# Optimization experiments

Hardware: AMD Instinct MI355X
Metric: run time of the kernel (lower is better)

The kernel has to match this reference:

```python
import jax, jax.numpy as jnp
import numpy as np

N, E, D, ED, L = 40000, 640000, 128, 16, 3  # nodes, edges, emb_dim, edge_dim, num_layer
BN_EPS = 1e-5


def setup_inputs() -> dict:
    key = jax.random.key(0)
    ks = jax.random.split(key, 20)
    s = 0.05
    inp = {
        "x": jax.random.normal(ks[0], (N, D), jnp.float32),
        "edge_attr": jax.random.normal(ks[1], (E, ED), jnp.float32),
        # node encoder Linear(input_dim, emb_dim)
        "node_W": jax.random.normal(ks[2], (D, D), jnp.float32) * s,
        "node_b": jnp.zeros((D,), jnp.float32),
        # per-layer params (leading dim L)
        "edge_W": jax.random.normal(ks[3], (L, ED, D), jnp.float32) * s,
        "edge_b": jnp.zeros((L, D), jnp.float32),
        "attn_W": jax.random.normal(ks[4], (L, 2 * D, 1), jnp.float32) * s,
        "attn_b": jnp.zeros((L, 1), jnp.float32),
        "eps": jnp.zeros((L,), jnp.float32),
        "W1": jax.random.normal(ks[5], (L, D, 2 * D), jnp.float32) * s,
        "b1": jnp.zeros((L, 2 * D), jnp.float32),
        "bn1_g": jnp.ones((L, 2 * D), jnp.float32),
        "bn1_b": jnp.zeros((L, 2 * D), jnp.float32),
        "W2": jax.random.normal(ks[6], (L, 2 * D, D), jnp.float32) * s,
        "b2": jnp.zeros((L, D), jnp.float32),
        "bn_g": jnp.ones((L, D), jnp.float32),
        "bn_b": jnp.zeros((L, D), jnp.float32),
        "edge_index": jax.random.randint(ks[7], (2, E), 0, N, jnp.int32),
    }
    return inp


def _bn_eval(h, g, b):
    # BatchNorm1d in eval with running_mean=0, running_var=1
    return g * h * (1.0 / np.sqrt(1.0 + BN_EPS)) + b


def reference(x, edge_attr, node_W, node_b, edge_W, edge_b, attn_W, attn_b,
              eps, W1, b1, bn1_g, bn1_b, W2, b2, bn_g, bn_b, edge_index):
    src, dst = edge_index[0], edge_index[1]
    h = x @ node_W + node_b  # node_encoder, [N, D]
    for l in range(L):
        e = edge_attr @ edge_W[l] + edge_b[l]       # [E, D] edge embedding
        xj = h[src]                                  # [E, D] source gather
        xi = h[dst]                                  # [E, D] target gather
        a = jax.nn.sigmoid(jnp.concatenate([xi, xj], axis=-1) @ attn_W[l] + attn_b[l])  # [E,1]
        msg = jax.nn.relu(xj * a + e)                # fused per-edge message
        agg = jax.ops.segment_sum(msg, dst, num_segments=N)  # scatter-add aggregate
        z = (1.0 + eps[l]) * h + agg
        # GIN mlp: Linear -> BN(eval) -> ReLU -> Linear
        z = _bn_eval(z @ W1[l] + b1[l], bn1_g[l], bn1_b[l])
        z = jax.nn.relu(z)
        z = z @ W2[l] + b2[l]
        # outer BatchNorm(eval); dropout = identity in eval; JK='last', no residual
        z = _bn_eval(z, bn_g[l], bn_b[l])
        if l < L - 1:
            z = jax.nn.relu(z)
        h = z
    return h
```

## Files before the change

kernel.cpp:

```cpp
#include <hip/hip_runtime.h>
#include <math.h>

#define NN 40000
#define EE 640000
#define DD 128
#define EDD 16
#define LL 3
#define TEB 64

__device__ __constant__ float kBnInv = 0.9999950000374997f;

typedef __bf16 bf16x8 __attribute__((ext_vector_type(8)));
typedef float  f32x4  __attribute__((ext_vector_type(4)));
typedef float  f32x2  __attribute__((ext_vector_type(2)));

__device__ __forceinline__ unsigned pack_bf2(float a, float b) {
    unsigned ua = __float_as_uint(a), ub = __float_as_uint(b);
    ua = (ua + 0x7fffu + ((ua >> 16) & 1u)) >> 16;
    ub = (ub + 0x7fffu + ((ub >> 16) & 1u)) & 0xffff0000u;
    return ua | ub;
}
__device__ __forceinline__ unsigned short bf16r(float x) {
    unsigned u = __float_as_uint(x);
    u = (u + 0x7fffu + ((u >> 16) & 1u)) >> 16;
    return (unsigned short)u;
}

__global__ __launch_bounds__(256) void node_enc_kernel(
    const float* __restrict__ x, const float* __restrict__ W,
    const float* __restrict__ b,
    const float* __restrict__ aW, const float* __restrict__ eps_p,
    float* __restrict__ h, unsigned* __restrict__ hb,
    float* __restrict__ pi, float* __restrict__ pj, float* __restrict__ z)
{
    __shared__ float xs[32][DD];
    const int t = threadIdx.x;
    const long rowbase = (long)blockIdx.x * 32;

    const float4* x4 = (const float4*)(x + rowbase * DD);
    float4* xs4 = (float4*)&xs[0][0];
#pragma unroll
    for (int i = 0; i < 4; i++) xs4[t + i * 256] = x4[t + i * 256];
    __syncthreads();

    const int c  = (t & 31) * 4;
    const int r0 = (t >> 5) * 4;

    float acc[4][4] = {};
    for (int k4 = 0; k4 < DD; k4 += 4) {
        float4 xr[4];
#pragma unroll
        for (int i = 0; i < 4; i++) xr[i] = *(const float4*)&xs[r0 + i][k4];
#pragma unroll
        for (int kk = 0; kk < 4; kk++) {
            const float4 w = *(const float4*)(W + (k4 + kk) * DD + c);
#pragma unroll
            for (int i = 0; i < 4; i++) {
                const float xv = ((const float*)&xr[i])[kk];
                acc[i][0] = fmaf(xv, w.x, acc[i][0]);
                acc[i][1] = fmaf(xv, w.y, acc[i][1]);
                acc[i][2] = fmaf(xv, w.z, acc[i][2]);
                acc[i][3] = fmaf(xv, w.w, acc[i][3]);
            }
        }
    }
    const float4 bv  = *(const float4*)(b + c);
    const float4 awi = *(const float4*)(aW + c);
    const float4 awj = *(const float4*)(aW + DD + c);
    const float ep = 1.0f + eps_p[0];

    float pa[4], pb[4];
#pragma unroll
    for (int i = 0; i < 4; i++) {
        const long row = rowbase + r0 + i;
        float4 ov = { acc[i][0] + bv.x, acc[i][1] + bv.y,
                      acc[i][2] + bv.z, acc[i][3] + bv.w };
        *(float4*)(h + row * DD + c) = ov;
        uint2 pv = { pack_bf2(ov.x, ov.y), pack_bf2(ov.z, ov.w) };
        *(uint2*)(hb + row * 64 + (c >> 1)) = pv;
        float4 zv = { ep * ov.x, ep * ov.y, ep * ov.z, ep * ov.w };
        *(float4*)(z + row * DD + c) = zv;
        pa[i] = ov.x * awi.x + ov.y * awi.y + ov.z * awi.z + ov.w * awi.w;
        pb[i] = ov.x * awj.x + ov.y * awj.y + ov.z * awj.z + ov.w * awj.w;
    }
#pragma unroll
    for (int off = 1; off < 32; off <<= 1) {
#pragma unroll
        for (int i = 0; i < 4; i++) {
            pa[i] += __shfl_xor(pa[i], off, 64);
            pb[i] += __shfl_xor(pb[i], off, 64);
        }
    }
    if ((t & 31) == 0) {
#pragma unroll
        for (int i = 0; i < 4; i++) {
            pi[rowbase + r0 + i] = pa[i];
            pj[rowbase + r0 + i] = pb[i];
        }
    }
}

__global__ __launch_bounds__(256) void wcast_kernel(
    const float* __restrict__ W1, const float* __restrict__ W2,
    unsigned short* __restrict__ w1t, unsigned short* __restrict__ w2t)
{
    const int idx = blockIdx.x * 256 + threadIdx.x;
    const int l = idx >> 15, r = idx & 32767;
    {   const int n = r >> 7, k = r & 127;
        w1t[idx] = bf16r(W1[(l << 15) + (k << 8) + n]);
    }
    {   const int n = r >> 8, k = r & 255;
        w2t[idx] = bf16r(W2[(l << 15) + (k << 7) + n]);
    }
}

__global__ __launch_bounds__(256) void hist_kernel(
    const int* __restrict__ edge_index, int* __restrict__ counts)
{
    const int i = blockIdx.x * 256 + threadIdx.x;
    atomicAdd(&counts[edge_index[EE + i]], 1);
}

__global__ __launch_bounds__(256) void scan1_kernel(
    const int* __restrict__ counts, int* __restrict__ scanned,
    int* __restrict__ partials)
{
    __shared__ int sdata[256];
    const int t = threadIdx.x;
    const int base = blockIdx.x * 1024 + t * 4;
    int v[4]; int sum = 0;
#pragma unroll
    for (int i = 0; i < 4; i++) {
        const int idx = base + i;
        v[i] = (idx < NN) ? counts[idx] : 0;
        sum += v[i];
    }
    sdata[t] = sum;
    __syncthreads();
    for (int off = 1; off < 256; off <<= 1) {
        int x = (t >= off) ? sdata[t - off] : 0;
        __syncthreads();
        sdata[t] += x;
        __syncthreads();
    }
    int run = sdata[t] - sum;
#pragma unroll
    for (int i = 0; i < 4; i++) {
        const int idx = base + i;
        if (idx < NN) scanned[idx] = run;
        run += v[i];
    }
    if (t == 255) partials[blockIdx.x] = sdata[255];
}

__global__ void scan2_kernel(int* __restrict__ partials)
{
    if (threadIdx.x == 0) {
        int run = 0;
        for (int i = 0; i < 40; i++) { int v = partials[i]; partials[i] = run; run += v; }
    }
}

__global__ __launch_bounds__(256) void scan3_kernel(
    const int* __restrict__ scanned, const int* __restrict__ partials,
    int* __restrict__ offsets, int* __restrict__ cursor)
{
    const int idx = blockIdx.x * 256 + threadIdx.x;
    if (idx < NN) {
        const int off = scanned[idx] + partials[idx >> 10];
        offsets[idx] = off;
        cursor[idx]  = off;
    }
}

__global__ __launch_bounds__(256) void scatter_kernel(
    const int* __restrict__ edge_index, const float* __restrict__ edge_attr,
    int* __restrict__ cursor,
    int* __restrict__ srcs_p, int* __restrict__ dstd_p,
    unsigned* __restrict__ ea_b)
{
    const int i = blockIdx.x * 256 + threadIdx.x;
    const int src = edge_index[i];
    const int dst = edge_index[EE + i];
    const int pos = atomicAdd(&cursor[dst], 1);
    srcs_p[pos] = src << 6;
    dstd_p[pos] = dst << 7;

    const float4* sp = (const float4*)(edge_attr + (long)i * EDD);
    const float4 s0 = sp[0], s1 = sp[1], s2 = sp[2], s3 = sp[3];
    uint4 o0 = { pack_bf2(s0.x, s0.y), pack_bf2(s0.z, s0.w),
                 pack_bf2(s1.x, s1.y), pack_bf2(s1.z, s1.w) };
    uint4 o1 = { pack_bf2(s2.x, s2.y), pack_bf2(s2.z, s2.w),
                 pack_bf2(s3.x, s3.y), pack_bf2(s3.z, s3.w) };
    *(uint4*)(ea_b + (long)pos * 8)     = o0;
    *(uint4*)(ea_b + (long)pos * 8 + 4) = o1;
}

__global__ __launch_bounds__(256) void edge_msg_kernel(
    const unsigned* __restrict__ hb, const unsigned* __restrict__ ea_b,
    const float* __restrict__ pi, const float* __restrict__ pj,
    const int* __restrict__ srcs_p, const int* __restrict__ dstd_p,
    const float* __restrict__ ab_p,
    const float* __restrict__ eW, const float* __restrict__ eb,
    float* __restrict__ z)
{
    __shared__ unsigned sh_hb[TEB * 64];
    __shared__ float    sh_ea[TEB * EDD];
    __shared__ int      sh_src[TEB];
    __shared__ int      sh_dst[TEB];
    __shared__ float    sh_a[TEB];

    const int t = threadIdx.x;
    const long e0 = (long)blockIdx.x * TEB;

    if (t < TEB) {
        const int ss = srcs_p[e0 + t];
        const int dd = dstd_p[e0 + t];
        sh_src[t] = ss;
        sh_dst[t] = dd;
        const float s = pi[dd >> 7] + pj[ss >> 6] + ab_p[0];
        sh_a[t] = 1.0f / (1.0f + expf(-s));
    }
    __syncthreads();

    {
        const int chunk = t & 15;
        const int r0    = t >> 4;
#pragma unroll
        for (int i = 0; i < TEB / 16; i++) {
            const int row  = r0 + 16 * i;
            const int srow = sh_src[row];
            *(uint4*)&sh_hb[row * 64 + chunk * 4] =
                *(const uint4*)(hb + srow + chunk * 4);
        }
#pragma unroll
        for (int i = 0; i < 2; i++) {
            const int idx  = t * 2 + i;
            const int edge = idx >> 3, q = idx & 7;
            const unsigned u = ea_b[e0 * 8 + idx];
            float2 f = { __uint_as_float(u << 16),
                         __uint_as_float(u & 0xffff0000u) };
            *(float2*)&sh_ea[edge * EDD + q * 2] = f;
        }
    }
    __syncthreads();

    const int wid = t >> 6, lane = t & 63;
    const int c0 = lane * 2;
    const int base = wid * (TEB / 4);

    f32x2 ew[EDD];
#pragma unroll
    for (int q = 0; q < EDD; q++) {
        const float2 w2 = ((const float2*)(eW + q * DD))[lane];
        ew[q][0] = w2.x; ew[q][1] = w2.y;
    }
    const float2 ebf = ((const float2*)eb)[lane];
    const f32x2 ebv = { ebf.x, ebf.y };
    const f32x2 zero2 = { 0.0f, 0.0f };

    f32x2 acc = zero2;
    int cur = sh_dst[base];

#pragma unroll 4
    for (int j = 0; j < TEB / 4; j++) {
        const int   dd = sh_dst[base + j];
        const float a  = sh_a[base + j];
        const unsigned u = sh_hb[(base + j) * 64 + lane];

        const float4* eap = (const float4*)&sh_ea[(base + j) * EDD];
        const float4 t0 = eap[0], t1 = eap[1], t2 = eap[2], t3 = eap[3];
        const float ea[EDD] = { t0.x,t0.y,t0.z,t0.w, t1.x,t1.y,t1.z,t1.w,
                                t2.x,t2.y,t2.z,t2.w, t3.x,t3.y,t3.z,t3.w };
        f32x2 ev = ebv;
#pragma unroll
        for (int q = 0; q < EDD; q++) {
            const f32x2 eaq = { ea[q], ea[q] };
            ev = __builtin_elementwise_fma(eaq, ew[q], ev);
        }

        if (dd != cur) {
            atomicAdd(&z[cur + c0],     acc[0]);
            atomicAdd(&z[cur + c0 + 1], acc[1]);
            acc = zero2; cur = dd;
        }
        const f32x2 xj = { __uint_as_float(u << 16),
                           __uint_as_float(u & 0xffff0000u) };
        const f32x2 av = { a, a };
        f32x2 m = __builtin_elementwise_fma(xj, av, ev);
        m = __builtin_elementwise_max(m, zero2);
        acc += m;
    }
    atomicAdd(&z[cur + c0],     acc[0]);
    atomicAdd(&z[cur + c0 + 1], acc[1]);
}

__global__ __launch_bounds__(256) void mlp_mfma_kernel(
    const float* __restrict__ zin,
    const unsigned short* __restrict__ w1t, const unsigned short* __restrict__ w2t,
    const float* __restrict__ b1, const float* __restrict__ g1, const float* __restrict__ bb1,
    const float* __restrict__ b2, const float* __restrict__ g2, const float* __restrict__ bb2,
    const float* __restrict__ aWn, const float* __restrict__ epsn_p,
    float* __restrict__ out, unsigned* __restrict__ hb,
    float* __restrict__ pi, float* __restrict__ pj, float* __restrict__ z,
    const int do_relu)
{
    __shared__ __align__(16) unsigned short zsb[64][136];
    __shared__ __align__(16) unsigned short usb[64][264];
    __shared__ float sh_pi[64], sh_pj[64];
    const int t = threadIdx.x;
    const int wid = t >> 6, lane = t & 63;
    const long rowbase = (long)blockIdx.x * 64;

    if (t < 64) { sh_pi[t] = 0.0f; sh_pj[t] = 0.0f; }

    {
        const float4* z4 = (const float4*)(zin + rowbase * DD);
#pragma unroll
        for (int i = 0; i < 8; i++) {
            const int idx = t + i * 256;
            const float4 v = z4[idx];
            const int row = idx >> 5;
            const int c4  = (idx & 31) * 4;
            uint2 pv = { pack_bf2(v.x, v.y), pack_bf2(v.z, v.w) };
            *(uint2*)&zsb[row][c4] = pv;
        }
    }
    __syncthreads();

    const int mrow  = lane & 15;
    const int quad  = lane >> 4;
    const f32x4 vzero = {0.0f, 0.0f, 0.0f, 0.0f};

    {
        const int nt0 = wid * 4;
        bf16x8 bf[4][4];
#pragma unroll
        for (int j = 0; j < 4; j++) {
            const unsigned short* wp = w1t + ((nt0 + j) * 16 + mrow) * 128 + quad * 8;
#pragma unroll
            for (int ks = 0; ks < 4; ks++)
                bf[j][ks] = *(const bf16x8*)(wp + ks * 32);
        }
        float gg[4], bi[4], bt[4];
#pragma unroll
        for (int j = 0; j < 4; j++) {
            const int c = (nt0 + j) * 16 + mrow;
            gg[j] = g1[c]; bi[j] = b1[c]; bt[j] = bb1[c];
        }
#pragma unroll
        for (int rt = 0; rt < 4; rt++) {
            bf16x8 af[4];
#pragma unroll
            for (int ks = 0; ks < 4; ks++)
                af[ks] = *(const bf16x8*)&zsb[rt * 16 + mrow][ks * 32 + quad * 8];
            f32x4 acc[4];
#pragma unroll
            for (int j = 0; j < 4; j++) acc[j] = vzero;
#pragma unroll
            for (int j = 0; j < 4; j++)
#pragma unroll
                for (int ks = 0; ks < 4; ks++)
                    acc[j] = __builtin_amdgcn_mfma_f32_16x16x32_bf16(af[ks], bf[j][ks], acc[j], 0, 0, 0);
#pragma unroll
            for (int j = 0; j < 4; j++) {
                const int c = (nt0 + j) * 16 + mrow;
#pragma unroll
                for (int r = 0; r < 4; r++) {
                    const int row = rt * 16 + quad * 4 + r;
                    const float u = fmaxf(fmaf(gg[j] * (acc[j][r] + bi[j]), kBnInv, bt[j]), 0.0f);
                    const float up = __shfl_xor(u, 1, 64);
                    if ((mrow & 1) == 0)
                        *(unsigned*)&usb[row][c] = pack_bf2(u, up);
                }
            }
        }
    }
    __syncthreads();

    {
        const int nt0 = wid * 2;
        bf16x8 bf[2][8];
#pragma unroll
        for (int j = 0; j < 2; j++) {
            const unsigned short* wp = w2t + ((nt0 + j) * 16 + mrow) * 256 + quad * 8;
#pragma unroll
            for (int ks = 0; ks < 8; ks++)
                bf[j][ks] = *(const bf16x8*)(wp + ks * 32);
        }
        float gg[2], bi[2], bt[2], awi[2], awj[2];
#pragma unroll
        for (int j = 0; j < 2; j++) {
            const int c = (nt0 + j) * 16 + mrow;
            gg[j] = g2[c]; bi[j] = b2[c]; bt[j] = bb2[c];
            awi[j] = aWn[c]; awj[j] = aWn[DD + c];
        }
        const float epn = do_relu ? (1.0f + epsn_p[0]) : 0.0f;

#pragma unroll
        for (int rt = 0; rt < 4; rt++) {
            bf16x8 af[8];
#pragma unroll
            for (int ks = 0; ks < 8; ks++)
                af[ks] = *(const bf16x8*)&usb[rt * 16 + mrow][ks * 32 + quad * 8];
            f32x4 acc[2];
            acc[0] = vzero; acc[1] = vzero;
#pragma unroll
            for (int j = 0; j < 2; j++)
#pragma unroll
                for (int ks = 0; ks < 8; ks++)
                    acc[j] = __builtin_amdgcn_mfma_f32_16x16x32_bf16(af[ks], bf[j][ks], acc[j], 0, 0, 0);

            float si[4] = {0, 0, 0, 0}, sj[4] = {0, 0, 0, 0};
#pragma unroll
            for (int j = 0; j < 2; j++) {
                const int c = (nt0 + j) * 16 + mrow;
#pragma unroll
                for (int r = 0; r < 4; r++) {
                    const long row = rowbase + rt * 16 + quad * 4 + r;
                    float v = fmaf(gg[j] * (acc[j][r] + bi[j]), kBnInv, bt[j]);
                    if (do_relu) {
                        v = fmaxf(v, 0.0f);
                        z[row * DD + c] = epn * v;
                        si[r] = fmaf(v, awi[j], si[r]);
                        sj[r] = fmaf(v, awj[j], sj[r]);
                    }
                    out[row * DD + c] = v;
                    const float vp = __shfl_xor(v, 1, 64);
                    if ((mrow & 1) == 0)
                        hb[row * 64 + (c >> 1)] = pack_bf2(v, vp);
                }
            }
            if (do_relu) {
#pragma unroll
                for (int off = 1; off < 16; off <<= 1) {
#pragma unroll
                    for (int r = 0; r < 4; r++) {
                        si[r] += __shfl_xor(si[r], off, 64);
                        sj[r] += __shfl_xor(sj[r], off, 64);
                    }
                }
                if (mrow == 0) {
#pragma unroll
                    for (int r = 0; r < 4; r++) {
                        atomicAdd(&sh_pi[rt * 16 + quad * 4 + r], si[r]);
                        atomicAdd(&sh_pj[rt * 16 + quad * 4 + r], sj[r]);
                    }
                }
            }
        }
    }
    if (do_relu) {
        __syncthreads();
        if (t < 64) {
            pi[rowbase + t] = sh_pi[t];
            pj[rowbase + t] = sh_pj[t];
        }
    }
}

extern "C" void kernel_launch(void* const* d_in, const int* in_sizes, int n_in,
                              void* d_out, int out_size, void* d_ws, size_t ws_size,
                              hipStream_t stream)
{
    const float* x         = (const float*)d_in[0];
    const float* edge_attr = (const float*)d_in[1];
    const float* node_W    = (const float*)d_in[2];
    const float* node_b    = (const float*)d_in[3];
    const float* edge_W    = (const float*)d_in[4];
    const float* edge_b    = (const float*)d_in[5];
    const float* attn_W    = (const float*)d_in[6];
    const float* attn_b    = (const float*)d_in[7];
    const float* eps       = (const float*)d_in[8];
    const float* W1        = (const float*)d_in[9];
    const float* b1        = (const float*)d_in[10];
    const float* bn1_g     = (const float*)d_in[11];
    const float* bn1_b     = (const float*)d_in[12];
    const float* W2        = (const float*)d_in[13];
    const float* b2        = (const float*)d_in[14];
    const float* bn_g      = (const float*)d_in[15];
    const float* bn_b      = (const float*)d_in[16];
    const int*   edge_index= (const int*)d_in[17];

    float* h    = (float*)d_ws;
    float* z    = h + (size_t)NN * DD;
    float* pi   = z + (size_t)NN * DD;
    float* pj   = pi + NN;
    unsigned* ea_b = (unsigned*)(pj + NN);
    unsigned* hbuf = ea_b + (size_t)EE * 8;
    unsigned short* w1t = (unsigned short*)(hbuf + (size_t)NN * 64);
    unsigned short* w2t = w1t + (size_t)LL * 32768;
    int* counts  = (int*)(w2t + (size_t)LL * 32768);
    int* offsets = counts + NN;
    int* cursor  = offsets + NN;
    int* scanned = cursor + NN;
    int* partials= scanned + 40960;
    int* srcs_p  = partials + 64;
    int* dstd_p  = srcs_p + EE;
    float* out = (float*)d_out;

    node_enc_kernel<<<NN / 32, 256, 0, stream>>>(
        x, node_W, node_b, attn_W, eps, h, hbuf, pi, pj, z);
    wcast_kernel<<<LL * 128, 256, 0, stream>>>(W1, W2, w1t, w2t);

    hipMemsetAsync(counts, 0, NN * sizeof(int), stream);
    hist_kernel<<<EE / 256, 256, 0, stream>>>(edge_index, counts);
    scan1_kernel<<<40, 256, 0, stream>>>(counts, scanned, partials);
    scan2_kernel<<<1, 64, 0, stream>>>(partials);
    scan3_kernel<<<(NN + 255) / 256, 256, 0, stream>>>(scanned, partials, offsets, cursor);
    scatter_kernel<<<EE / 256, 256, 0, stream>>>(
        edge_index, edge_attr, cursor, srcs_p, dstd_p, ea_b);

    for (int l = 0; l < LL; l++) {
        const int ln = (l + 1 < LL) ? (l + 1) : l;
        edge_msg_kernel<<<EE / TEB, 256, 0, stream>>>(
            hbuf, ea_b, pi, pj, srcs_p, dstd_p, attn_b + l,
            edge_W + (size_t)l * EDD * DD, edge_b + (size_t)l * DD, z);
        mlp_mfma_kernel<<<NN / 64, 256, 0, stream>>>(
            z,
            w1t + (size_t)l * 32768, w2t + (size_t)l * 32768,
            b1 + (size_t)l * 2 * DD, bn1_g + (size_t)l * 2 * DD, bn1_b + (size_t)l * 2 * DD,
            b2 + (size_t)l * DD, bn_g + (size_t)l * DD, bn_b + (size_t)l * DD,
            attn_W + (size_t)ln * 2 * DD, eps + ln,
            (l == LL - 1) ? out : h, hbuf, pi, pj, z, (l < LL - 1) ? 1 : 0);
    }
}
```

Baseline: 522.5 us.

## Keep edge attrs fp32 with uniform loads, drop unused fp32 h writes

Stops writing the fp32 node features h, which only the final layer's output needs, and skips writing hb in the last layer. Edge attributes are now stored permuted in fp32 instead of bf16 and read directly from global memory with wave-uniform addresses (readfirstlane), replacing the shared-memory staging. dst and attention values are read as vectors from shared memory. The trade is double the edge-attr bytes per layer in exchange for fewer writes, less LDS traffic and one less conversion.

```diff
diff --git a/kernel.cpp b/kernel.cpp
--- a/kernel.cpp
+++ b/kernel.cpp
@@ -30,7 +30,7 @@
     const float* __restrict__ x, const float* __restrict__ W,
     const float* __restrict__ b,
     const float* __restrict__ aW, const float* __restrict__ eps_p,
-    float* __restrict__ h, unsigned* __restrict__ hb,
+    unsigned* __restrict__ hb,
     float* __restrict__ pi, float* __restrict__ pj, float* __restrict__ z)
 {
     __shared__ float xs[32][DD];
@@ -75,7 +75,6 @@
         const long row = rowbase + r0 + i;
         float4 ov = { acc[i][0] + bv.x, acc[i][1] + bv.y,
                       acc[i][2] + bv.z, acc[i][3] + bv.w };
-        *(float4*)(h + row * DD + c) = ov;
         uint2 pv = { pack_bf2(ov.x, ov.y), pack_bf2(ov.z, ov.w) };
         *(uint2*)(hb + row * 64 + (c >> 1)) = pv;
         float4 zv = { ep * ov.x, ep * ov.y, ep * ov.z, ep * ov.w };
@@ -177,7 +176,7 @@
     const int* __restrict__ edge_index, const float* __restrict__ edge_attr,
     int* __restrict__ cursor,
     int* __restrict__ srcs_p, int* __restrict__ dstd_p,
-    unsigned* __restrict__ ea_b)
+    float* __restrict__ ea_p)
 {
     const int i = blockIdx.x * 256 + threadIdx.x;
     const int src = edge_index[i];
@@ -187,17 +186,12 @@
     dstd_p[pos] = dst << 7;
 
     const float4* sp = (const float4*)(edge_attr + (long)i * EDD);
-    const float4 s0 = sp[0], s1 = sp[1], s2 = sp[2], s3 = sp[3];
-    uint4 o0 = { pack_bf2(s0.x, s0.y), pack_bf2(s0.z, s0.w),
-                 pack_bf2(s1.x, s1.y), pack_bf2(s1.z, s1.w) };
-    uint4 o1 = { pack_bf2(s2.x, s2.y), pack_bf2(s2.z, s2.w),
-                 pack_bf2(s3.x, s3.y), pack_bf2(s3.z, s3.w) };
-    *(uint4*)(ea_b + (long)pos * 8)     = o0;
-    *(uint4*)(ea_b + (long)pos * 8 + 4) = o1;
+    float4* dp = (float4*)(ea_p + (long)pos * EDD);
+    dp[0] = sp[0]; dp[1] = sp[1]; dp[2] = sp[2]; dp[3] = sp[3];
 }
 
 __global__ __launch_bounds__(256) void edge_msg_kernel(
-    const unsigned* __restrict__ hb, const unsigned* __restrict__ ea_b,
+    const unsigned* __restrict__ hb, const float* __restrict__ ea_p,
     const float* __restrict__ pi, const float* __restrict__ pj,
     const int* __restrict__ srcs_p, const int* __restrict__ dstd_p,
     const float* __restrict__ ab_p,
@@ -205,10 +199,9 @@
     float* __restrict__ z)
 {
     __shared__ unsigned sh_hb[TEB * 64];
-    __shared__ float    sh_ea[TEB * EDD];
     __shared__ int      sh_src[TEB];
-    __shared__ int      sh_dst[TEB];
-    __shared__ float    sh_a[TEB];
+    __shared__ __align__(16) int   sh_dst[TEB];
+    __shared__ __align__(16) float sh_a[TEB];
 
     const int t = threadIdx.x;
     const long e0 = (long)blockIdx.x * TEB;
@@ -233,15 +226,6 @@
             *(uint4*)&sh_hb[row * 64 + chunk * 4] =
                 *(const uint4*)(hb + srow + chunk * 4);
         }
-#pragma unroll
-        for (int i = 0; i < 2; i++) {
-            const int idx  = t * 2 + i;
-            const int edge = idx >> 3, q = idx & 7;
-            const unsigned u = ea_b[e0 * 8 + idx];
-            float2 f = { __uint_as_float(u << 16),
-                         __uint_as_float(u & 0xffff0000u) };
-            *(float2*)&sh_ea[edge * EDD + q * 2] = f;
-        }
     }
     __syncthreads();
 
@@ -261,35 +245,41 @@
 
     f32x2 acc = zero2;
     int cur = sh_dst[base];
-
-#pragma unroll 4
-    for (int j = 0; j < TEB / 4; j++) {
-        const int   dd = sh_dst[base + j];
-        const float a  = sh_a[base + j];
-        const unsigned u = sh_hb[(base + j) * 64 + lane];
-
-        const float4* eap = (const float4*)&sh_ea[(base + j) * EDD];
-        const float4 t0 = eap[0], t1 = eap[1], t2 = eap[2], t3 = eap[3];
-        const float ea[EDD] = { t0.x,t0.y,t0.z,t0.w, t1.x,t1.y,t1.z,t1.w,
-                                t2.x,t2.y,t2.z,t2.w, t3.x,t3.y,t3.z,t3.w };
-        f32x2 ev = ebv;
-#pragma unroll
-        for (int q = 0; q < EDD; q++) {
-            const f32x2 eaq = { ea[q], ea[q] };
-            ev = __builtin_elementwise_fma(eaq, ew[q], ev);
-        }
-
-        if (dd != cur) {
-            atomicAdd(&z[cur + c0],     acc[0]);
-            atomicAdd(&z[cur + c0 + 1], acc[1]);
-            acc = zero2; cur = dd;
-        }
-        const f32x2 xj = { __uint_as_float(u << 16),
-                           __uint_as_float(u & 0xffff0000u) };
-        const f32x2 av = { a, a };
-        f32x2 m = __builtin_elementwise_fma(xj, av, ev);
-        m = __builtin_elementwise_max(m, zero2);
-        acc += m;
+    const int ebase_s = __builtin_amdgcn_readfirstlane((int)e0 + base);
+
+#pragma unroll 2
+    for (int j4 = 0; j4 < TEB / 4; j4 += 4) {
+        const int4   dd4 = *(const int4*)&sh_dst[base + j4];
+        const float4 aa4 = *(const float4*)&sh_a[base + j4];
+        const int   dd[4] = { dd4.x, dd4.y, dd4.z, dd4.w };
+        const float aa[4] = { aa4.x, aa4.y, aa4.z, aa4.w };
+#pragma unroll
+        for (int r = 0; r < 4; r++) {
+            const int j = j4 + r;
+            const unsigned u = sh_hb[(base + j) * 64 + lane];
+            const float4* eap = (const float4*)(ea_p + (long)(ebase_s + j) * EDD);
+            const float4 t0 = eap[0], t1 = eap[1], t2 = eap[2], t3 = eap[3];
+            const float ea[EDD] = { t0.x,t0.y,t0.z,t0.w, t1.x,t1.y,t1.z,t1.w,
+                                    t2.x,t2.y,t2.z,t2.w, t3.x,t3.y,t3.z,t3.w };
+            f32x2 ev = ebv;
+#pragma unroll
+            for (int q = 0; q < EDD; q++) {
+                const f32x2 eaq = { ea[q], ea[q] };
+                ev = __builtin_elementwise_fma(eaq, ew[q], ev);
+            }
+
+            if (dd[r] != cur) {
+                atomicAdd(&z[cur + c0],     acc[0]);
+                atomicAdd(&z[cur + c0 + 1], acc[1]);
+                acc = zero2; cur = dd[r];
+            }
+            const f32x2 xj = { __uint_as_float(u << 16),
+                               __uint_as_float(u & 0xffff0000u) };
+            const f32x2 av = { aa[r], aa[r] };
+            f32x2 m = __builtin_elementwise_fma(xj, av, ev);
+            m = __builtin_elementwise_max(m, zero2);
+            acc += m;
+        }
     }
     atomicAdd(&z[cur + c0],     acc[0]);
     atomicAdd(&z[cur + c0 + 1], acc[1]);
@@ -424,11 +414,12 @@
                         z[row * DD + c] = epn * v;
                         si[r] = fmaf(v, awi[j], si[r]);
                         sj[r] = fmaf(v, awj[j], sj[r]);
+                        const float vp = __shfl_xor(v, 1, 64);
+                        if ((mrow & 1) == 0)
+                            hb[row * 64 + (c >> 1)] = pack_bf2(v, vp);
+                    } else {
+                        out[row * DD + c] = v;
                     }
-                    out[row * DD + c] = v;
-                    const float vp = __shfl_xor(v, 1, 64);
-                    if ((mrow & 1) == 0)
-                        hb[row * 64 + (c >> 1)] = pack_bf2(v, vp);
                 }
             }
             if (do_relu) {
@@ -482,12 +473,12 @@
     const float* bn_b      = (const float*)d_in[16];
     const int*   edge_index= (const int*)d_in[17];
 
-    float* h    = (float*)d_ws;
-    float* z    = h + (size_t)NN * DD;
+    float* dummy = (float*)d_ws;
+    float* z    = dummy + (size_t)NN * DD;
     float* pi   = z + (size_t)NN * DD;
     float* pj   = pi + NN;
-    unsigned* ea_b = (unsigned*)(pj + NN);
-    unsigned* hbuf = ea_b + (size_t)EE * 8;
+    float* ea_p = pj + NN;
+    unsigned* hbuf = (unsigned*)(ea_p + (size_t)EE * EDD);
     unsigned short* w1t = (unsigned short*)(hbuf + (size_t)NN * 64);
     unsigned short* w2t = w1t + (size_t)LL * 32768;
     int* counts  = (int*)(w2t + (size_t)LL * 32768);
@@ -500,7 +491,7 @@
     float* out = (float*)d_out;
 
     node_enc_kernel<<<NN / 32, 256, 0, stream>>>(
-        x, node_W, node_b, attn_W, eps, h, hbuf, pi, pj, z);
+        x, node_W, node_b, attn_W, eps, hbuf, pi, pj, z);
     wcast_kernel<<<LL * 128, 256, 0, stream>>>(W1, W2, w1t, w2t);
 
     hipMemsetAsync(counts, 0, NN * sizeof(int), stream);
@@ -509,12 +500,12 @@
     scan2_kernel<<<1, 64, 0, stream>>>(partials);
     scan3_kernel<<<(NN + 255) / 256, 256, 0, stream>>>(scanned, partials, offsets, cursor);
     scatter_kernel<<<EE / 256, 256, 0, stream>>>(
-        edge_index, edge_attr, cursor, srcs_p, dstd_p, ea_b);
+        edge_index, edge_attr, cursor, srcs_p, dstd_p, ea_p);
 
     for (int l = 0; l < LL; l++) {
         const int ln = (l + 1 < LL) ? (l + 1) : l;
         edge_msg_kernel<<<EE / TEB, 256, 0, stream>>>(
-            hbuf, ea_b, pi, pj, srcs_p, dstd_p, attn_b + l,
+            hbuf, ea_p, pi, pj, srcs_p, dstd_p, attn_b + l,
             edge_W + (size_t)l * EDD * DD, edge_b + (size_t)l * DD, z);
         mlp_mfma_kernel<<<NN / 64, 256, 0, stream>>>(
             z,
@@ -522,6 +513,6 @@
             b1 + (size_t)l * 2 * DD, bn1_g + (size_t)l * 2 * DD, bn1_b + (size_t)l * 2 * DD,
             b2 + (size_t)l * DD, bn_g + (size_t)l * DD, bn_b + (size_t)l * DD,
             attn_W + (size_t)ln * 2 * DD, eps + ln,
-            (l == LL - 1) ? out : h, hbuf, pi, pj, z, (l < LL - 1) ? 1 : 0);
-    }
-}
+            (l == LL - 1) ? out : dummy, hbuf, pi, pj, z, (l < LL - 1) ? 1 : 0);
+    }
+}
```

Result: slower. 550.3 us (+5.3%).
